# Kernel optimization log

Measured on AMD Instinct MI355X. Metric: run time of the kernel, lower is better.

The kernel has to match this reference:

```python
import jax, jax.numpy as jnp
import numpy as np

TEMPERATURE = 1.0
WEIGHT = 1.0


def _transitivity_sum(rel):
    """rel: [N, N] relation probabilities for one (batch, relation) slice.
    Computes sum_{a,b,c} relu(rel[a,b] - rel[a,c] * rel[b,c]) via a scan over c
    (outer product of column c), keeping memory at O(N^2) instead of O(N^3)."""
    def step(acc, col):  # col = rel[:, c], shape [N]
        viol = jax.nn.relu(rel - col[:, None] * col[None, :])  # [N, N]
        return acc + jnp.sum(viol), None
    acc, _ = jax.lax.scan(step, jnp.zeros((), rel.dtype), rel.T)
    return acc


def setup_inputs() -> dict:
    key = jax.random.key(0)
    B, N, R = 2, 512, 4
    relation_logits = jax.random.normal(key, (B, N, N, R), dtype=jnp.float32)
    entity_masks = jnp.ones((B, N), dtype=jnp.int32)
    return {"relation_logits": relation_logits, "entity_masks": entity_masks}


def reference(relation_logits, entity_masks):
    B, N, _, R = relation_logits.shape
    probs = jax.nn.sigmoid(relation_logits / TEMPERATURE)  # [B, N, N, R]
    m = (entity_masks > 0).astype(probs.dtype)             # [B, N]
    rel = probs * m[:, :, None, None] * m[:, None, :, None]
    # flatten (batch, relation) and vmap the per-matrix cubic reduction
    rel_br = jnp.transpose(rel, (0, 3, 1, 2)).reshape(B * R, N, N)
    per = jax.vmap(_transitivity_sum)(rel_br)              # [B*R]
    # per-batch loss = sum_r / R; final = weight * mean over batch
    return WEIGHT * jnp.sum(per) / (R * B)
```

## Files before the change

kernel.cpp:

```cpp
#include <hip/hip_runtime.h>
#include <math.h>

#define N      512
#define RNUM   4
#define BNUM   2
#define NSLICE (RNUM * BNUM)
#define TILE   128
#define CT     64
#define CSPLIT 8
#define NCOLB  16
#define SCALE  0.0625f

typedef _Float16 half2_t __attribute__((ext_vector_type(2)));

__device__ __forceinline__ unsigned int h2u(half2_t h) {
  return __builtin_bit_cast(unsigned int, h);
}
__device__ __forceinline__ half2_t u2h(unsigned int u) {
  return __builtin_bit_cast(half2_t, u);
}

__device__ __forceinline__ float sigmoidf_(float x) {
  return __builtin_amdgcn_rcpf(1.0f + __expf(-x));
}

__global__ void zero_out_kernel(float* out) { out[0] = 0.0f; }

__global__ __launch_bounds__(256) void prep_f16_kernel(const float* __restrict__ logits,
                                                       const int* __restrict__ masks,
                                                       _Float16* __restrict__ P,
                                                       float* __restrict__ out) {
  if (blockIdx.x == 0 && threadIdx.x == 0) out[0] = 0.0f;
  int t = blockIdx.x * 256 + threadIdx.x;
  int b = t >> 18;
  int rem = t & (N * N - 1);
  int i = rem >> 9;
  int j = rem & (N - 1);
  float4 lg = *(const float4*)(logits + (size_t)t * 4);
  float mm = ((masks[b * N + i] > 0) && (masks[b * N + j] > 0)) ? 1.0f : 0.0f;
  size_t base = (size_t)b * RNUM * N * N + rem;
  P[base + 0 * (size_t)N * N] = (_Float16)(mm * sigmoidf_(lg.x));
  P[base + 1 * (size_t)N * N] = (_Float16)(mm * sigmoidf_(lg.y));
  P[base + 2 * (size_t)N * N] = (_Float16)(mm * sigmoidf_(lg.z));
  P[base + 3 * (size_t)N * N] = (_Float16)(mm * sigmoidf_(lg.w));
}

__global__ __launch_bounds__(256, 2) void work_f16_kernel(const _Float16* __restrict__ P,
                                                          float* __restrict__ out) {
  __shared__ __align__(16) _Float16 tA[128 * CT];
  __shared__ __align__(16) _Float16 tB[128 * CT];
  __shared__ float wsum[4];

  const int tid = threadIdx.x;
  const int bid = blockIdx.x;

  if (bid < NCOLB) {
    const int s    = bid >> 1;
    const int half = bid & 1;
    const int c    = half * 256 + tid;
    const _Float16* col = P + (size_t)s * N * N + c;
    float sum = 0.0f;
#pragma unroll 8
    for (int a = 0; a < N; ++a) sum += (float)col[(size_t)a * N];
    float v = sum * ((float)N - sum);
    for (int off = 32; off > 0; off >>= 1) v += __shfl_down(v, off, 64);
    const int wid = tid >> 6;
    if ((tid & 63) == 0) wsum[wid] = v;
    __syncthreads();
    if (tid == 0)
      atomicAdd(out, (wsum[0] + wsum[1] + wsum[2] + wsum[3]) * SCALE);
    return;
  }

  const int m  = bid - NCOLB;
  const int bt = m & 3;
  const int at = (m >> 2) & 3;
  const int s  = (m >> 4) & 7;
  const int cz = m >> 7;
  const int a0 = at * TILE;
  const int b0 = bt * TILE;
  const int c0 = cz * CT;

  const int ta = tid & 15;
  const int tb = tid >> 4;

  const _Float16* Ph = P + (size_t)s * N * N;

  half2_t bc[8][8];
#pragma unroll
  for (int x = 0; x < 8; ++x) {
    int ga = a0 + ((x >> 2) << 6) + (ta << 2) + (x & 3);
    const _Float16* rrow = Ph + (size_t)ga * N + b0;
    uint2 u0 = *(const uint2*)(rrow + (tb << 2));
    uint2 u1 = *(const uint2*)(rrow + 64 + (tb << 2));
    half2_t p0 = u2h(u0.x), p1 = u2h(u0.y), p2 = u2h(u1.x), p3 = u2h(u1.y);
    bc[x][0] = half2_t{p0.x, p0.x};
    bc[x][1] = half2_t{p0.y, p0.y};
    bc[x][2] = half2_t{p1.x, p1.x};
    bc[x][3] = half2_t{p1.y, p1.y};
    bc[x][4] = half2_t{p2.x, p2.x};
    bc[x][5] = half2_t{p2.y, p2.y};
    bc[x][6] = half2_t{p3.x, p3.x};
    bc[x][7] = half2_t{p3.y, p3.y};
  }

  {
    const int sx   = tid & 127;
    const int sarr = tid >> 7;
    const _Float16* srow = Ph + (size_t)((sarr ? b0 : a0) + sx) * N + c0;
    _Float16* dst = (sarr ? tB : tA) + sx * CT;
    const int key = (sx >> 2) & 7;
    const uint4* src = (const uint4*)srow;
#pragma unroll
    for (int cbg = 0; cbg < 8; ++cbg) {
      uint4 q = src[cbg];
      *(uint4*)&dst[(cbg ^ key) << 3] = q;
    }
  }
  __syncthreads();

  half2_t acc2[8][2];
#pragma unroll
  for (int x = 0; x < 8; ++x) { acc2[x][0] = u2h(0u); acc2[x][1] = u2h(0u); }

  const int keyA = ta & 7;
  const int keyB = tb & 7;
  int arow[8], brow[8];
#pragma unroll
  for (int x = 0; x < 8; ++x)
    arow[x] = (((x >> 2) << 6) | (ta << 2) | (x & 3)) * CT;
#pragma unroll
  for (int y = 0; y < 8; ++y)
    brow[y] = (((y >> 2) << 6) | (tb << 2) | (y & 3)) * CT;

#pragma unroll 1
  for (int cb = 0; cb < 8; ++cb) {
    uint4 bq[8];
#pragma unroll
    for (int y = 0; y < 8; ++y)
      bq[y] = *(const uint4*)&tB[brow[y] + ((cb ^ keyB) << 3)];
#pragma unroll
    for (int x = 0; x < 8; ++x) {
      uint4 aq = *(const uint4*)&tA[arow[x] + ((cb ^ keyA) << 3)];
      unsigned int au[4] = {aq.x, aq.y, aq.z, aq.w};
#pragma unroll
      for (int y = 0; y < 8; ++y) {
        unsigned int bu[4] = {bq[y].x, bq[y].y, bq[y].z, bq[y].w};
#pragma unroll
        for (int k = 0; k < 4; ++k) {
          half2_t t2 = __builtin_elementwise_fma(-u2h(au[k]), u2h(bu[k]),
                                                 bc[x][y]);
          acc2[x][y & 1] += u2h(h2u(t2) & 0x7FFF7FFFu);
        }
      }
    }
  }

  float tsum = 0.0f;
#pragma unroll
  for (int x = 0; x < 8; ++x) {
    tsum += (float)acc2[x][0].x + (float)acc2[x][0].y +
            (float)acc2[x][1].x + (float)acc2[x][1].y;
  }

  for (int off = 32; off > 0; off >>= 1) tsum += __shfl_down(tsum, off, 64);

  const int wid = tid >> 6;
  if ((tid & 63) == 0) wsum[wid] = tsum;
  __syncthreads();
  if (tid == 0)
    atomicAdd(out, (wsum[0] + wsum[1] + wsum[2] + wsum[3]) * SCALE);
}

#define FCT    64
#define FSTR   132
#define FCSPL  4

__global__ __launch_bounds__(256, 2) void work_f32_fallback(const float* __restrict__ logits,
                                                            const int* __restrict__ masks,
                                                            float* __restrict__ out) {
  __shared__ __align__(16) float tAf[FCT][FSTR];
  __shared__ __align__(16) float tBf[FCT][FSTR];
  __shared__ float wsum[4];

  const int tid = threadIdx.x;
  const int bid = blockIdx.x;

  if (bid < NCOLB) {
    const int s    = bid >> 1;
    const int half = bid & 1;
    const int c    = half * 256 + tid;
    const int bb   = s >> 2;
    const int r    = s & 3;
    const int* mrow = masks + bb * N;
    float mc = (mrow[c] > 0) ? 1.0f : 0.0f;
    float sum = 0.0f;
#pragma unroll 4
    for (int a = 0; a < N; ++a) {
      float ma = (mrow[a] > 0) ? 1.0f : 0.0f;
      size_t idx = ((size_t)(bb * N + a) * N + c) * RNUM + r;
      sum += sigmoidf_(logits[idx]) * ma * mc;
    }
    float v = sum * ((float)N - sum);
    for (int off = 32; off > 0; off >>= 1) v += __shfl_down(v, off, 64);
    const int wid = tid >> 6;
    if ((tid & 63) == 0) wsum[wid] = v;
    __syncthreads();
    if (tid == 0)
      atomicAdd(out, (wsum[0] + wsum[1] + wsum[2] + wsum[3]) * SCALE);
    return;
  }

  const int m  = bid - NCOLB;
  const int bt = m & 3;
  const int at = (m >> 2) & 3;
  const int s  = (m >> 4) & 7;
  const int cz = m >> 7;
  const int a0 = at * TILE;
  const int b0 = bt * TILE;
  const int bb = s >> 2;
  const int r  = s & 3;
  const int cbeg = cz * (N / FCSPL);
  const int cend = cbeg + (N / FCSPL);

  const int ta = tid & 15;
  const int tb = tid >> 4;
  const int* mrow = masks + bb * N;

  float rab[8][8];
#pragma unroll
  for (int x = 0; x < 8; ++x) {
    int ra = a0 + ((x >> 2) << 6) + ta * 4 + (x & 3);
    float ma = (mrow[ra] > 0) ? 1.0f : 0.0f;
#pragma unroll
    for (int y = 0; y < 8; ++y) {
      int cb = b0 + ((y >> 2) << 6) + tb * 4 + (y & 3);
      float mb = (mrow[cb] > 0) ? 1.0f : 0.0f;
      size_t idx = ((size_t)(bb * N + ra) * N + cb) * RNUM + r;
      rab[x][y] = sigmoidf_(logits[idx]) * ma * mb;
    }
  }

  float acc[8][2];
#pragma unroll
  for (int x = 0; x < 8; ++x) { acc[x][0] = 0.0f; acc[x][1] = 0.0f; }

  for (int c0 = cbeg; c0 < cend; c0 += FCT) {
    __syncthreads();
#pragma unroll
    for (int it = 0; it < 32; ++it) {
      int e = it * 256 + tid;
      int c = e & 63;
      int i = e >> 6;
      int pc = ((((i >> 2) ^ ((c >> 2) & 31)) & 31) << 2) | (i & 3);
      float mc = (mrow[c0 + c] > 0) ? 1.0f : 0.0f;
      {
        float mi = (mrow[a0 + i] > 0) ? 1.0f : 0.0f;
        size_t idx = ((size_t)(bb * N + a0 + i) * N + (c0 + c)) * RNUM + r;
        tAf[c][pc] = sigmoidf_(logits[idx]) * mi * mc;
      }
      {
        float mi = (mrow[b0 + i] > 0) ? 1.0f : 0.0f;
        size_t idx = ((size_t)(bb * N + b0 + i) * N + (c0 + c)) * RNUM + r;
        tBf[c][pc] = sigmoidf_(logits[idx]) * mi * mc;
      }
    }
    __syncthreads();

#pragma unroll 2
    for (int cg = 0; cg < FCT / 4; ++cg) {
      const float* pa = &tAf[cg * 4][((ta ^ cg) & 31) << 2];
      const float* pb = &tBf[cg * 4][((tb ^ cg) & 31) << 2];
#pragma unroll
      for (int dc = 0; dc < 4; ++dc) {
        float4 a0v = *(const float4*)(pa + dc * FSTR);
        float4 a1v = *(const float4*)(pa + dc * FSTR + 64);
        float4 b0v = *(const float4*)(pb + dc * FSTR);
        float4 b1v = *(const float4*)(pb + dc * FSTR + 64);
        float avv[8] = {a0v.x, a0v.y, a0v.z, a0v.w, a1v.x, a1v.y, a1v.z, a1v.w};
        float bvv[8] = {b0v.x, b0v.y, b0v.z, b0v.w, b1v.x, b1v.y, b1v.z, b1v.w};
#pragma unroll
        for (int x = 0; x < 8; ++x) {
#pragma unroll
          for (int y = 0; y < 4; ++y)
            acc[x][0] += fabsf(fmaf(-avv[x], bvv[y], rab[x][y]));
#pragma unroll
          for (int y = 4; y < 8; ++y)
            acc[x][1] += fabsf(fmaf(-avv[x], bvv[y], rab[x][y]));
        }
      }
    }
  }

  float tsum = 0.0f;
#pragma unroll
  for (int x = 0; x < 8; ++x) tsum += acc[x][0] + acc[x][1];
  for (int off = 32; off > 0; off >>= 1) tsum += __shfl_down(tsum, off, 64);
  const int wid = tid >> 6;
  if ((tid & 63) == 0) wsum[wid] = tsum;
  __syncthreads();
  if (tid == 0)
    atomicAdd(out, (wsum[0] + wsum[1] + wsum[2] + wsum[3]) * SCALE);
}

extern "C" void kernel_launch(void* const* d_in, const int* in_sizes, int n_in,
                              void* d_out, int out_size, void* d_ws, size_t ws_size,
                              hipStream_t stream) {
  const float* logits = (const float*)d_in[0];
  const int*   masks  = (const int*)d_in[1];
  float*       out    = (float*)d_out;

  const size_t P_BYTES = (size_t)NSLICE * N * N * sizeof(_Float16);

  if (ws_size >= P_BYTES) {
    _Float16* P = (_Float16*)d_ws;
    prep_f16_kernel<<<(BNUM * N * N) / 256, 256, 0, stream>>>(logits, masks, P, out);
    const int nblocks = NCOLB + 4 * 4 * NSLICE * CSPLIT;
    work_f16_kernel<<<nblocks, 256, 0, stream>>>(P, out);
  } else {
    zero_out_kernel<<<1, 1, 0, stream>>>(out);
    const int nblocks = NCOLB + 4 * 4 * NSLICE * FCSPL;
    work_f32_fallback<<<nblocks, 256, 0, stream>>>(logits, masks, out);
  }
}
```

Baseline: 117.4 us.

## Process two c-chunks per block with register prefetch and vectorize f16 prep stores

Each work block now covers two 64-wide c chunks instead of one, halving the block count. This amortizes the per-block setup of the broadcast register tile bc, which is reloaded from global memory per block. Both chunks' shared-memory tiles are prefetched into registers before the bc load to overlap global latency, and partial half sums are flushed to fp32 accumulators per chunk. The prep kernel handles two j per thread with packed half2 stores, at the cost of more register pressure and fewer blocks to fill the GPU.

Result: slower. 130.2 us (+10.9%).

```diff
diff --git a/kernel.cpp b/kernel.cpp
--- a/kernel.cpp
+++ b/kernel.cpp
@@ -7,7 +7,8 @@
 #define NSLICE (RNUM * BNUM)
 #define TILE   128
 #define CT     64
-#define CSPLIT 8
+#define NCH    2
+#define CSPLIT 4
 #define NCOLB  16
 #define SCALE  0.0625f
 
@@ -32,17 +33,28 @@
                                                        float* __restrict__ out) {
   if (blockIdx.x == 0 && threadIdx.x == 0) out[0] = 0.0f;
   int t = blockIdx.x * 256 + threadIdx.x;
-  int b = t >> 18;
-  int rem = t & (N * N - 1);
-  int i = rem >> 9;
-  int j = rem & (N - 1);
-  float4 lg = *(const float4*)(logits + (size_t)t * 4);
-  float mm = ((masks[b * N + i] > 0) && (masks[b * N + j] > 0)) ? 1.0f : 0.0f;
-  size_t base = (size_t)b * RNUM * N * N + rem;
-  P[base + 0 * (size_t)N * N] = (_Float16)(mm * sigmoidf_(lg.x));
-  P[base + 1 * (size_t)N * N] = (_Float16)(mm * sigmoidf_(lg.y));
-  P[base + 2 * (size_t)N * N] = (_Float16)(mm * sigmoidf_(lg.z));
-  P[base + 3 * (size_t)N * N] = (_Float16)(mm * sigmoidf_(lg.w));
+  int b = t >> 17;
+  int rem = t & ((N * N / 2) - 1);
+  int i = rem >> 8;
+  int jp = rem & ((N / 2) - 1);
+  int j = jp << 1;
+  const float* lg = logits + ((size_t)((b * N + i) * N + j)) * RNUM;
+  float4 l0 = *(const float4*)(lg);
+  float4 l1 = *(const float4*)(lg + RNUM);
+  const int* mrow = masks + b * N;
+  float mi = (mrow[i] > 0) ? 1.0f : 0.0f;
+  float m0 = mi * ((mrow[j] > 0) ? 1.0f : 0.0f);
+  float m1 = mi * ((mrow[j + 1] > 0) ? 1.0f : 0.0f);
+  size_t base = (size_t)b * RNUM * N * N + (size_t)i * N + j;
+  float v0[4] = {l0.x, l0.y, l0.z, l0.w};
+  float v1[4] = {l1.x, l1.y, l1.z, l1.w};
+#pragma unroll
+  for (int r = 0; r < RNUM; ++r) {
+    half2_t h;
+    h.x = (_Float16)(m0 * sigmoidf_(v0[r]));
+    h.y = (_Float16)(m1 * sigmoidf_(v1[r]));
+    *(unsigned int*)(P + base + (size_t)r * N * N) = h2u(h);
+  }
 }
 
 __global__ __launch_bounds__(256, 2) void work_f16_kernel(const _Float16* __restrict__ P,
@@ -79,12 +91,26 @@
   const int cz = m >> 7;
   const int a0 = at * TILE;
   const int b0 = bt * TILE;
-  const int c0 = cz * CT;
+  const int c0 = cz * (CT * NCH);
 
   const int ta = tid & 15;
   const int tb = tid >> 4;
 
   const _Float16* Ph = P + (size_t)s * N * N;
+
+  const int sx   = tid & 127;
+  const int sarr = tid >> 7;
+  const _Float16* srow = Ph + (size_t)((sarr ? b0 : a0) + sx) * N + c0;
+  _Float16* dst = (sarr ? tB : tA) + sx * CT;
+  const int key = (sx >> 2) & 7;
+  uint4 q0v[8], q1v[8];
+  {
+    const uint4* src = (const uint4*)srow;
+#pragma unroll
+    for (int g = 0; g < 8; ++g) q0v[g] = src[g];
+#pragma unroll
+    for (int g = 0; g < 8; ++g) q1v[g] = src[8 + g];
+  }
 
   half2_t bc[8][8];
 #pragma unroll
@@ -104,25 +130,6 @@
     bc[x][7] = half2_t{p3.y, p3.y};
   }
 
-  {
-    const int sx   = tid & 127;
-    const int sarr = tid >> 7;
-    const _Float16* srow = Ph + (size_t)((sarr ? b0 : a0) + sx) * N + c0;
-    _Float16* dst = (sarr ? tB : tA) + sx * CT;
-    const int key = (sx >> 2) & 7;
-    const uint4* src = (const uint4*)srow;
-#pragma unroll
-    for (int cbg = 0; cbg < 8; ++cbg) {
-      uint4 q = src[cbg];
-      *(uint4*)&dst[(cbg ^ key) << 3] = q;
-    }
-  }
-  __syncthreads();
-
-  half2_t acc2[8][2];
-#pragma unroll
-  for (int x = 0; x < 8; ++x) { acc2[x][0] = u2h(0u); acc2[x][1] = u2h(0u); }
-
   const int keyA = ta & 7;
   const int keyB = tb & 7;
   int arow[8], brow[8];
@@ -133,35 +140,60 @@
   for (int y = 0; y < 8; ++y)
     brow[y] = (((y >> 2) << 6) | (tb << 2) | (y & 3)) * CT;
 
+  float acc[8];
+#pragma unroll
+  for (int x = 0; x < 8; ++x) acc[x] = 0.0f;
+
+  for (int ch = 0; ch < NCH; ++ch) {
+    if (ch == 0) {
+#pragma unroll
+      for (int g = 0; g < 8; ++g)
+        *(uint4*)&dst[(g ^ key) << 3] = q0v[g];
+    } else {
+      __syncthreads();
+#pragma unroll
+      for (int g = 0; g < 8; ++g)
+        *(uint4*)&dst[(g ^ key) << 3] = q1v[g];
+    }
+    __syncthreads();
+
+    half2_t acc2[8][2];
+#pragma unroll
+    for (int x = 0; x < 8; ++x) { acc2[x][0] = u2h(0u); acc2[x][1] = u2h(0u); }
+
 #pragma unroll 1
-  for (int cb = 0; cb < 8; ++cb) {
-    uint4 bq[8];
-#pragma unroll
-    for (int y = 0; y < 8; ++y)
-      bq[y] = *(const uint4*)&tB[brow[y] + ((cb ^ keyB) << 3)];
-#pragma unroll
-    for (int x = 0; x < 8; ++x) {
-      uint4 aq = *(const uint4*)&tA[arow[x] + ((cb ^ keyA) << 3)];
-      unsigned int au[4] = {aq.x, aq.y, aq.z, aq.w};
-#pragma unroll
-      for (int y = 0; y < 8; ++y) {
-        unsigned int bu[4] = {bq[y].x, bq[y].y, bq[y].z, bq[y].w};
-#pragma unroll
-        for (int k = 0; k < 4; ++k) {
-          half2_t t2 = __builtin_elementwise_fma(-u2h(au[k]), u2h(bu[k]),
-                                                 bc[x][y]);
-          acc2[x][y & 1] += u2h(h2u(t2) & 0x7FFF7FFFu);
+    for (int cb = 0; cb < 8; ++cb) {
+      uint4 bq[8];
+#pragma unroll
+      for (int y = 0; y < 8; ++y)
+        bq[y] = *(const uint4*)&tB[brow[y] + ((cb ^ keyB) << 3)];
+#pragma unroll
+      for (int x = 0; x < 8; ++x) {
+        uint4 aq = *(const uint4*)&tA[arow[x] + ((cb ^ keyA) << 3)];
+        unsigned int au[4] = {aq.x, aq.y, aq.z, aq.w};
+#pragma unroll
+        for (int y = 0; y < 8; ++y) {
+          unsigned int bu[4] = {bq[y].x, bq[y].y, bq[y].z, bq[y].w};
+#pragma unroll
+          for (int k = 0; k < 4; ++k) {
+            half2_t t2 = __builtin_elementwise_fma(-u2h(au[k]), u2h(bu[k]),
+                                                   bc[x][y]);
+            acc2[x][y & 1] += u2h(h2u(t2) & 0x7FFF7FFFu);
+          }
         }
       }
     }
+
+#pragma unroll
+    for (int x = 0; x < 8; ++x) {
+      acc[x] += (float)acc2[x][0].x + (float)acc2[x][0].y +
+                (float)acc2[x][1].x + (float)acc2[x][1].y;
+    }
   }
 
   float tsum = 0.0f;
 #pragma unroll
-  for (int x = 0; x < 8; ++x) {
-    tsum += (float)acc2[x][0].x + (float)acc2[x][0].y +
-            (float)acc2[x][1].x + (float)acc2[x][1].y;
-  }
+  for (int x = 0; x < 8; ++x) tsum += acc[x];
 
   for (int off = 32; off > 0; off >>= 1) tsum += __shfl_down(tsum, off, 64);
 
@@ -314,7 +346,7 @@
 
   if (ws_size >= P_BYTES) {
     _Float16* P = (_Float16*)d_ws;
-    prep_f16_kernel<<<(BNUM * N * N) / 256, 256, 0, stream>>>(logits, masks, P, out);
+    prep_f16_kernel<<<(BNUM * N * N / 2) / 256, 256, 0, stream>>>(logits, masks, P, out);
     const int nblocks = NCOLB + 4 * 4 * NSLICE * CSPLIT;
     work_f16_kernel<<<nblocks, 256, 0, stream>>>(P, out);
   } else {
```
